# Kernel optimization log

Hardware: AMD Instinct MI355X
Metric: run time of the kernel (lower is better)

## Reference

```python
import jax, jax.numpy as jnp
import numpy as np
import math

DIM = 2048
NUM_HEADS = 16
HEAD_DIM = DIM // NUM_HEADS
SEQ = 2048
BATCH = 4
THETA = 10000.0


def _rope_tables(seq_len, d, theta):
    # faithful to RotaryEmbedding: emb = cat([freqs, freqs], -1), then [..., ::2]
    inv_freq = 1.0 / theta ** (np.arange(0, d, 2, dtype=np.float32) / d)  # [d/2]
    t = np.arange(seq_len, dtype=np.float32)
    freqs = np.einsum('i,j->ij', t, inv_freq)          # [S, d/2]
    emb = np.concatenate([freqs, freqs], axis=-1)       # [S, d]
    cos_split = np.cos(emb)[:, ::2]                     # [S, d/2]
    sin_split = np.sin(emb)[:, ::2]                     # [S, d/2]
    return jnp.asarray(cos_split), jnp.asarray(sin_split)


def _apply_rope(x, cos_s, sin_s):
    # x: [b, h, s, d]; cos_s/sin_s: [s, d/2]
    x1 = x[..., ::2]
    x2 = x[..., 1::2]
    c = cos_s[None, None]
    s = sin_s[None, None]
    return jnp.concatenate([x1 * c - x2 * s, x1 * s + x2 * c], axis=-1)


def setup_inputs() -> dict:
    key = jax.random.key(0)
    k1, k2, k3 = jax.random.split(key, 3)
    x = jax.random.normal(k1, (BATCH, SEQ, DIM), dtype=jnp.float32)
    # causal additive mask [1,1,S,S]
    neg = jnp.finfo(jnp.float32).min
    causal = jnp.tril(jnp.ones((SEQ, SEQ), dtype=bool))
    mask = jnp.where(causal, 0.0, neg)[None, None].astype(jnp.float32)
    w_qkv = jax.random.normal(k2, (3 * DIM, DIM), dtype=jnp.float32) * (1.0 / math.sqrt(DIM))
    w_out = jax.random.normal(k3, (DIM, DIM), dtype=jnp.float32) * (1.0 / math.sqrt(DIM))
    return {"x": x, "mask": mask, "w_qkv": w_qkv, "w_out": w_out}


def reference(x, mask, w_qkv, w_out):
    b, s, _ = x.shape
    h, d = NUM_HEADS, HEAD_DIM
    qkv = jnp.einsum('bse,fe->bsf', x, w_qkv)           # [b, s, 3*dim]
    q, k, v = jnp.split(qkv, 3, axis=-1)
    # b s (h d) -> b h s d
    reshp = lambda t: t.reshape(b, s, h, d).transpose(0, 2, 1, 3)
    q, k, v = reshp(q), reshp(k), reshp(v)
    cos_s, sin_s = _rope_tables(s, d, THETA)
    q = _apply_rope(q, cos_s, sin_s)
    k = _apply_rope(k, cos_s, sin_s)
    att = jnp.einsum('bhqd,bhkd->bhqk', q, k) / math.sqrt(d)
    att = att + mask
    att = jax.nn.softmax(att, axis=-1)
    y = jnp.einsum('bhqk,bhkd->bhqd', att, v)           # [b, h, s, d]
    y = y.transpose(0, 2, 1, 3).reshape(b, s, h * d)
    return jnp.einsum('bse,fe->bsf', y, w_out)
```

## Files before the change

kernel.cpp:

```cpp
#include <hip/hip_runtime.h>

typedef unsigned short u16;
typedef unsigned int u32;
typedef __attribute__((ext_vector_type(4))) float f32x4;
typedef __attribute__((ext_vector_type(16))) float f32x16;
typedef __attribute__((ext_vector_type(8))) short bf16x8;
typedef __attribute__((ext_vector_type(4))) float float4v;
typedef __attribute__((ext_vector_type(4))) unsigned short u16x4;
typedef __attribute__((ext_vector_type(8))) unsigned short u16x8;

__device__ __forceinline__ float bf2f(u16 u) { return __uint_as_float(((u32)u) << 16); }
__device__ __forceinline__ u16 f2bf(float f) {
  u32 x = __float_as_uint(f);
  x += 0x7fffu + ((x >> 16) & 1u);
  return (u16)(x >> 16);
}
__device__ __forceinline__ u32 cvtpk(float lo, float hi_) {
  u32 r;
  asm("v_cvt_pk_bf16_f32 %0, %1, %2" : "=v"(r) : "v"(lo), "v"(hi_));
  return r;
}

__device__ __forceinline__ void gll16(const void* g, void* l) {
  __builtin_amdgcn_global_load_lds((const __attribute__((address_space(1))) void*)g,
                                   (__attribute__((address_space(3))) void*)l, 16, 0, 0);
}

#define MFMA_BF16(a, b, c) __builtin_amdgcn_mfma_f32_16x16x32_bf16((a), (b), (c), 0, 0, 0)
#define MFMA32(a, b, c) __builtin_amdgcn_mfma_f32_32x32x16_bf16((a), (b), (c), 0, 0, 0)

#define BARRIER() __builtin_amdgcn_s_barrier()
#define VMCNT(n) asm volatile("s_waitcnt vmcnt(" #n ")" ::: "memory")

__global__ __launch_bounds__(256) void cast_kernel(const float* __restrict__ src,
                                                   u16* __restrict__ dst, int n) {
  const int stride = gridDim.x * 256 * 4;
  for (int i = (blockIdx.x * 256 + threadIdx.x) * 4; i < n; i += stride) {
    const float4v v = *(const float4v*)(src + i);
    u16x4 o;
    o[0] = f2bf(v[0]); o[1] = f2bf(v[1]); o[2] = f2bf(v[2]); o[3] = f2bf(v[3]);
    *(u16x4*)(dst + i) = o;
  }
}

__global__ __launch_bounds__(256) void rope_tables(float* __restrict__ cosd,
                                                   float* __restrict__ sind) {
  const int idx = blockIdx.x * 256 + threadIdx.x;
  const int t = idx >> 6, j = idx & 63;
  const float inv = powf(10000.0f, -(float)(j & 31) * (1.0f / 32.0f));
  const float ang = (float)t * inv;
  cosd[idx] = cosf(ang);
  sind[idx] = sinf(ang);
}

#define PH_MFMA(MG, NG, BF)                                                      \
  do {                                                                           \
    _Pragma("unroll") for (int i_ = 0; i_ < 4; ++i_)                             \
      _Pragma("unroll") for (int jn_ = 0; jn_ < 2; ++jn_)                        \
        _Pragma("unroll") for (int ks_ = 0; ks_ < 2; ++ks_)                      \
          acc[(MG) * 4 + i_][(NG) * 2 + jn_] =                                   \
              MFMA_BF16(af[i_][ks_], BF[jn_][ks_],                               \
                        acc[(MG) * 4 + i_][(NG) * 2 + jn_]);                     \
  } while (0)

#define LDB_M(bb, ng, BF)                                                        \
  do {                                                                           \
    const char* base_ = (const char*)&LDS[bb][1][ng][0];                         \
    _Pragma("unroll") for (int jn_ = 0; jn_ < 2; ++jn_) {                        \
      const int R_ = jn_ * 64 + wc * 16 + l15;                                   \
      _Pragma("unroll") for (int ks_ = 0; ks_ < 2; ++ks_)                        \
        BF[jn_][ks_] = *(const bf16x8*)(base_ + R_ * 128 +                       \
                                        ((ks_ * 64 + l4 * 16) ^ ((R_ & 7) << 4)));\
    }                                                                            \
  } while (0)

template <int MODE>
__global__ __launch_bounds__(512, 2) void gemm_bt8(const u16* __restrict__ A,
                                                   const u16* __restrict__ B,
                                                   void* __restrict__ Cv, int M, int N, int K,
                                                   int lda, int ldb, int ldc) {
  __shared__ __align__(16) u16 LDS[2][2][2][128 * 64];
  const int nbn = N >> 8;
  const int nwg = gridDim.x;
  const int wg = (blockIdx.x & 7) * (nwg >> 3) + (blockIdx.x >> 3);
  const int bm = wg / nbn, bn = wg % nbn;
  const int tid = threadIdx.x;
  const int w = tid >> 6, l = tid & 63, l15 = l & 15, l4 = l >> 4;
  const int wr = w >> 2, wc = w & 3;
  const u16* Abase = A + (size_t)bm * 256 * lda;
  const u16* Bbase = B + (size_t)bn * 256 * ldb;
  const int NT = K >> 6;

  f32x4 acc[8][4] = {};
  bf16x8 af[4][2], bfr0[2][2], bfr1[2][2];

  auto STAGE = [&](int sel, int h, int t) {
    const u16* src = (sel ? Bbase + (size_t)h * 128 * ldb : Abase + (size_t)h * 128 * lda) +
                     t * 64;
    const int ld = sel ? ldb : lda;
    char* dst = (char*)&LDS[t & 1][sel][h][0];
#pragma unroll
    for (int j = 0; j < 2; ++j) {
      const int o = j * 8192 + tid * 16;
      const int r = o >> 7;
      const int cb = (o & 127) ^ ((r & 7) << 4);
      gll16(src + (size_t)r * ld + (cb >> 1), dst + o);
    }
  };
  auto LDA_ = [&](int bb, int mg) {
    const char* base = (const char*)&LDS[bb][0][mg][0];
#pragma unroll
    for (int i = 0; i < 4; ++i) {
      const int R = i * 32 + wr * 16 + l15;
#pragma unroll
      for (int ks = 0; ks < 2; ++ks)
        af[i][ks] = *(const bf16x8*)(base + R * 128 + ((ks * 64 + l4 * 16) ^ ((R & 7) << 4)));
    }
  };

  STAGE(0, 0, 0); STAGE(1, 0, 0); STAGE(0, 1, 0); STAGE(1, 1, 0);
  if (NT > 1) { STAGE(1, 0, 1); STAGE(1, 1, 1); STAGE(0, 1, 1); }
  VMCNT(6);
  BARRIER();

  for (int T = 0; T < NT; ++T) {
    const int bb = T & 1;
    LDA_(bb, 0); LDB_M(bb, 0, bfr0);
    if (T + 1 < NT) STAGE(0, 0, T + 1);
    BARRIER();
    __builtin_amdgcn_s_setprio(1); PH_MFMA(0, 0, bfr0); __builtin_amdgcn_s_setprio(0);
    BARRIER();
    LDB_M(bb, 1, bfr1);
    if (T + 2 < NT) STAGE(1, 0, T + 2);
    BARRIER();
    __builtin_amdgcn_s_setprio(1); PH_MFMA(0, 1, bfr1); __builtin_amdgcn_s_setprio(0);
    BARRIER();
    LDA_(bb, 1);
    if (T + 2 < NT) STAGE(1, 1, T + 2);
    BARRIER();
    __builtin_amdgcn_s_setprio(1); PH_MFMA(1, 1, bfr1); __builtin_amdgcn_s_setprio(0);
    BARRIER();
    if (T + 2 < NT) STAGE(0, 1, T + 2);
    BARRIER();
    __builtin_amdgcn_s_setprio(1); PH_MFMA(1, 0, bfr0); __builtin_amdgcn_s_setprio(0);
    if (T + 2 < NT) { VMCNT(6); } else { VMCNT(0); }
    BARRIER();
  }

#pragma unroll
  for (int mf = 0; mf < 8; ++mf) {
    const int mg = mf >> 2, i = mf & 3;
    const int row0 = bm * 256 + mg * 128 + i * 32 + wr * 16 + l4 * 4;
#pragma unroll
    for (int f = 0; f < 4; ++f) {
      const int col = bn * 256 + f * 64 + wc * 16 + l15;
      const f32x4 a = acc[mf][f];
      if (MODE == 0) {
        float* C = (float*)Cv;
#pragma unroll
        for (int r = 0; r < 4; ++r)
          C[(size_t)(row0 + r) * ldc + col] = a[r];
      } else if (bn < 16) {
        u16* C = (u16*)Cv;
#pragma unroll
        for (int r = 0; r < 4; ++r)
          C[(size_t)(row0 + r) * 6144 + col] = f2bf(a[r]);
      } else {
        u16* C = (u16*)Cv;
        const int batch = row0 >> 11;
        const int s0 = row0 & 2047;
        const int vcol = col - 4096;
        u16* vb = C + (size_t)((batch * 16 + (vcol >> 7)) * 128 + (vcol & 127)) * 6144 +
                  4096 + s0;
        union { u32 u[2]; u16x4 v; } pk;
        pk.u[0] = cvtpk(a[0], a[1]);
        pk.u[1] = cvtpk(a[2], a[3]);
        *(u16x4*)vb = pk.v;
      }
    }
  }
}

__global__ __launch_bounds__(256) void rope_apply_inplace(u16* __restrict__ qkvb,
                                                          const float* __restrict__ cosd,
                                                          const float* __restrict__ sind) {
  const int wid = blockIdx.x * 4 + (threadIdx.x >> 6);
  const int j = threadIdx.x & 63;
  const int h = wid & 15;
  const int m = wid >> 4;
  const int s = m & 2047;
  const float c = cosd[s * 64 + j];
  const float sn = sind[s * 64 + j];
  u16* qp = qkvb + (size_t)m * 6144 + h * 128;
  u16* kp = qp + 2048;
  const u32 qv = *(const u32*)(qp + 2 * j);
  const u32 kv = *(const u32*)(kp + 2 * j);
  const float q1 = bf2f((u16)(qv & 0xffff)), q2 = bf2f((u16)(qv >> 16));
  const float k1 = bf2f((u16)(kv & 0xffff)), k2 = bf2f((u16)(kv >> 16));
  qp[j]      = f2bf(q1 * c - q2 * sn);
  qp[64 + j] = f2bf(q1 * sn + q2 * c);
  kp[j]      = f2bf(k1 * c - k2 * sn);
  kp[64 + j] = f2bf(k1 * sn + k2 * c);
}

__global__ __launch_bounds__(512, 2) void flash_attn(u16* __restrict__ qkvb) {
  __shared__ __align__(16) char smem[65536];
  const int bh = blockIdx.x;
  const int qt = 7 - blockIdx.y;
  const int b = bh >> 4, h = bh & 15;
  const int tid = threadIdx.x;
  const int w = tid >> 6, l = tid & 63;
  const int l31 = l & 31, hi = l >> 5;

  const int q0 = qt * 256 + w * 32;
  const int qg = q0 + l31;

  bf16x8 qf[8];
  {
    const u16* Qrow = qkvb + (size_t)(b * 2048 + qg) * 6144 + h * 128 + hi * 8;
#pragma unroll
    for (int d = 0; d < 8; ++d) qf[d] = *(const bf16x8*)(Qrow + d * 16);
  }

  f32x16 ot[4];
#pragma unroll
  for (int dt = 0; dt < 4; ++dt) ot[dt] = 0.f;
  float mrun = -1e30f, lrun = 0.f;

  const int NT = 4 * qt + 4;
  const u16* Kg0 = qkvb + (size_t)b * 2048 * 6144 + 2048 + h * 128;
  const u16* Vg0 = qkvb + (size_t)bh * 128 * 6144 + 4096;

  auto STAGE = [&](int t) {
    const u16* Kg = Kg0 + (size_t)t * 64 * 6144;
    const u16* Vg = Vg0 + t * 64;
    char* kd = smem + (t & 1) * 16384;
    char* vd = smem + 32768 + (t & 1) * 16384;
#pragma unroll
    for (int j = 0; j < 2; ++j) {
      const int o = j * 8192 + tid * 16;
      {
        const int r = o >> 8;
        const int cb = (o & 255) ^ ((r & 15) << 4);
        gll16(Kg + (size_t)r * 6144 + (cb >> 1), kd + o);
      }
      {
        const int r = o >> 7;
        const int cb = (o & 127) ^ ((r & 7) << 4);
        gll16(Vg + (size_t)r * 6144 + (cb >> 1), vd + o);
      }
    }
  };

  STAGE(0);
  VMCNT(0);
  BARRIER();

  for (int kt = 0; kt < NT; ++kt) {
    if (kt + 1 < NT) STAGE(kt + 1);

    if (kt * 64 <= q0 + 31) {
      const char* Kb = smem + (kt & 1) * 16384;
      const char* Vb = smem + 32768 + (kt & 1) * 16384;

      f32x16 sa[2];
      sa[0] = 0.f; sa[1] = 0.f;
#pragma unroll
      for (int ks2 = 0; ks2 < 2; ++ks2) {
        const int R = ks2 * 32 + l31;
#pragma unroll
        for (int d = 0; d < 8; ++d) {
          const bf16x8 kf = *(const bf16x8*)(Kb + R * 256 +
                                             ((d * 32 + hi * 16) ^ ((R & 15) << 4)));
          sa[ks2] = MFMA32(kf, qf[d], sa[ks2]);
        }
      }

      const float SCALE = 0.08838834764831845f;
      float tmax = -1e30f;
      if (kt * 64 + 63 > q0) {
#pragma unroll
        for (int ks2 = 0; ks2 < 2; ++ks2)
#pragma unroll
          for (int rg = 0; rg < 16; ++rg) {
            const int key = kt * 64 + ks2 * 32 + (rg & 3) + 8 * (rg >> 2) + 4 * hi;
            float sv = sa[ks2][rg] * SCALE;
            sv = (key > qg) ? -1e30f : sv;
            sa[ks2][rg] = sv;
            tmax = fmaxf(tmax, sv);
          }
      } else {
#pragma unroll
        for (int ks2 = 0; ks2 < 2; ++ks2)
#pragma unroll
          for (int rg = 0; rg < 16; ++rg) {
            const float sv = sa[ks2][rg] * SCALE;
            sa[ks2][rg] = sv;
            tmax = fmaxf(tmax, sv);
          }
      }
      tmax = fmaxf(tmax, __shfl_xor(tmax, 32));

      const float mnew = fmaxf(mrun, tmax);
      const float alpha = __expf(mrun - mnew);
      mrun = mnew;
      float rsum = 0.f;
#pragma unroll
      for (int ks2 = 0; ks2 < 2; ++ks2)
#pragma unroll
        for (int rg = 0; rg < 16; ++rg) {
          const float pv = __expf(sa[ks2][rg] - mnew);
          sa[ks2][rg] = pv;
          rsum += pv;
        }
      rsum += __shfl_xor(rsum, 32);
      lrun = lrun * alpha + rsum;
#pragma unroll
      for (int dt = 0; dt < 4; ++dt)
#pragma unroll
        for (int rg = 0; rg < 16; ++rg) ot[dt][rg] *= alpha;

      bf16x8 pfrag[4];
#pragma unroll
      for (int t = 0; t < 4; ++t) {
        const int ks2 = t >> 1;
        const int gA = 2 * (t & 1);
        const int gB = gA + 1;
        const u32 a0 = cvtpk(sa[ks2][gA * 4 + 0], sa[ks2][gA * 4 + 1]);
        const u32 a1 = cvtpk(sa[ks2][gA * 4 + 2], sa[ks2][gA * 4 + 3]);
        const u32 b0 = cvtpk(sa[ks2][gB * 4 + 0], sa[ks2][gB * 4 + 1]);
        const u32 b1 = cvtpk(sa[ks2][gB * 4 + 2], sa[ks2][gB * 4 + 3]);
        const u32 snd0 = hi ? a0 : b0;
        const u32 snd1 = hi ? a1 : b1;
        const u32 rcv0 = (u32)__shfl_xor((int)snd0, 32);
        const u32 rcv1 = (u32)__shfl_xor((int)snd1, 32);
        union { u32 u[4]; bf16x8 v; } pk;
        pk.u[0] = hi ? rcv0 : a0;
        pk.u[1] = hi ? rcv1 : a1;
        pk.u[2] = hi ? b0 : rcv0;
        pk.u[3] = hi ? b1 : rcv1;
        pfrag[t] = pk.v;
      }

#pragma unroll
      for (int dt = 0; dt < 4; ++dt) {
        const int R = dt * 32 + l31;
#pragma unroll
        for (int t = 0; t < 4; ++t) {
          const bf16x8 vf = *(const bf16x8*)(Vb + R * 128 +
                                             ((t * 32 + hi * 16) ^ ((R & 7) << 4)));
          ot[dt] = MFMA32(vf, pfrag[t], ot[dt]);
        }
      }
    }

    VMCNT(0);
    BARRIER();
  }

  const float inv = 1.0f / lrun;
  char* E = smem + w * 8192;
#pragma unroll
  for (int dt = 0; dt < 4; ++dt)
#pragma unroll
    for (int rp = 0; rp < 8; ++rp) {
      const int rg = 2 * rp;
      const int d0 = dt * 32 + (rg & 3) + 8 * (rg >> 2) + 4 * hi;
      const u32 pkv = cvtpk(ot[dt][rg] * inv, ot[dt][rg + 1] * inv);
      *(u32*)(E + l31 * 256 + ((d0 * 2) ^ ((l31 & 15) << 4))) = pkv;
    }
#pragma unroll
  for (int p = 0; p < 8; ++p) {
    const int q = p * 4 + (l >> 4);
    const int c = l & 15;
    const bf16x8 vv = *(const bf16x8*)(E + q * 256 + ((c * 16) ^ ((q & 15) << 4)));
    *(bf16x8*)(qkvb + (size_t)(b * 2048 + q0 + q) * 6144 + h * 128 + c * 8) = vv;
  }
}

extern "C" void kernel_launch(void* const* d_in, const int* in_sizes, int n_in,
                              void* d_out, int out_size, void* d_ws, size_t ws_size,
                              hipStream_t stream) {
  const float* x     = (const float*)d_in[0];
  const float* w_qkv = (const float*)d_in[2];
  const float* w_out = (const float*)d_in[3];
  float* out = (float*)d_out;
  char* ws = (char*)d_ws;

  u16* woutb = (u16*)(ws);
  u16* xb    = (u16*)(ws + ((size_t)8 << 20));
  u16* wqkvb = (u16*)(ws + ((size_t)40 << 20));
  u16* qkvb  = (u16*)(ws + ((size_t)64 << 20));
  float* cosd = (float*)(ws + ((size_t)160 << 20));
  float* sind = (float*)(ws + ((size_t)160 << 20) + ((size_t)1 << 19));

  cast_kernel<<<2048, 256, 0, stream>>>(x, xb, 8192 * 2048);
  cast_kernel<<<2048, 256, 0, stream>>>(w_qkv, wqkvb, 6144 * 2048);
  cast_kernel<<<1024, 256, 0, stream>>>(w_out, woutb, 2048 * 2048);
  rope_tables<<<512, 256, 0, stream>>>(cosd, sind);
  gemm_bt8<1><<<768, 512, 0, stream>>>(xb, wqkvb, qkvb, 8192, 6144, 2048,
                                       2048, 2048, 6144);
  rope_apply_inplace<<<32768, 256, 0, stream>>>(qkvb, cosd, sind);
  flash_attn<<<dim3(64, 8), 512, 0, stream>>>(qkvb);
  gemm_bt8<0><<<256, 512, 0, stream>>>(qkvb, woutb, out, 8192, 2048, 2048,
                                       6144, 2048, 2048);
}
```

Before: 415.1 us.

## Fuse RoPE into QKV GEMM epilogue and unroll K loop by two

Removes the separate rope_apply_inplace kernel and applies the rotary embedding in the QKV GEMM epilogue, using a lane shuffle to pair even and odd columns and writing the results into the split-half layout. The GEMM main loop is also unrolled by two k-tiles, so LDS buffer indices are compile-time constants rather than computed from T&1. This saves a full read-modify-write pass over Q and K, at the cost of scattered epilogue stores and cos/sin loads inside the GEMM. The unrolled loop and the unconditional prologue assume NT is even and at least 2.

```diff
diff --git a/kernel.cpp b/kernel.cpp
--- a/kernel.cpp
+++ b/kernel.cpp
@@ -30,6 +30,7 @@
 #define MFMA32(a, b, c) __builtin_amdgcn_mfma_f32_32x32x16_bf16((a), (b), (c), 0, 0, 0)
 
 #define BARRIER() __builtin_amdgcn_s_barrier()
+#define SETP(n) __builtin_amdgcn_s_setprio(n)
 #define VMCNT(n) asm volatile("s_waitcnt vmcnt(" #n ")" ::: "memory")
 
 __global__ __launch_bounds__(256) void cast_kernel(const float* __restrict__ src,
@@ -74,11 +75,30 @@
     }                                                                            \
   } while (0)
 
+#define KTILE(BB, OB, TT)                                                        \
+  do {                                                                           \
+    LDA_(BB, 0); LDB_M(BB, 0, bfr0);                                            \
+    if ((TT) + 1 < NT) STAGE(OB, 0, 0, (TT) + 1);                                \
+    BARRIER(); SETP(1); PH_MFMA(0, 0, bfr0); SETP(0); BARRIER();                 \
+    LDB_M(BB, 1, bfr1);                                                          \
+    if ((TT) + 2 < NT) STAGE(BB, 1, 0, (TT) + 2);                                \
+    BARRIER(); SETP(1); PH_MFMA(0, 1, bfr1); SETP(0); BARRIER();                 \
+    LDA_(BB, 1);                                                                 \
+    if ((TT) + 2 < NT) STAGE(BB, 1, 1, (TT) + 2);                                \
+    BARRIER(); SETP(1); PH_MFMA(1, 1, bfr1); SETP(0); BARRIER();                 \
+    if ((TT) + 2 < NT) STAGE(BB, 0, 1, (TT) + 2);                                \
+    BARRIER(); SETP(1); PH_MFMA(1, 0, bfr0); SETP(0);                            \
+    if ((TT) + 2 < NT) { VMCNT(6); } else { VMCNT(0); }                          \
+    BARRIER();                                                                   \
+  } while (0)
+
 template <int MODE>
 __global__ __launch_bounds__(512, 2) void gemm_bt8(const u16* __restrict__ A,
                                                    const u16* __restrict__ B,
                                                    void* __restrict__ Cv, int M, int N, int K,
-                                                   int lda, int ldb, int ldc) {
+                                                   int lda, int ldb, int ldc,
+                                                   const float* __restrict__ cosd,
+                                                   const float* __restrict__ sind) {
   __shared__ __align__(16) u16 LDS[2][2][2][128 * 64];
   const int nbn = N >> 8;
   const int nwg = gridDim.x;
@@ -94,11 +114,11 @@
   f32x4 acc[8][4] = {};
   bf16x8 af[4][2], bfr0[2][2], bfr1[2][2];
 
-  auto STAGE = [&](int sel, int h, int t) {
+  auto STAGE = [&](int buf, int sel, int h, int t) {
     const u16* src = (sel ? Bbase + (size_t)h * 128 * ldb : Abase + (size_t)h * 128 * lda) +
                      t * 64;
     const int ld = sel ? ldb : lda;
-    char* dst = (char*)&LDS[t & 1][sel][h][0];
+    char* dst = (char*)&LDS[buf][sel][h][0];
 #pragma unroll
     for (int j = 0; j < 2; ++j) {
       const int o = j * 8192 + tid * 16;
@@ -118,33 +138,14 @@
     }
   };
 
-  STAGE(0, 0, 0); STAGE(1, 0, 0); STAGE(0, 1, 0); STAGE(1, 1, 0);
-  if (NT > 1) { STAGE(1, 0, 1); STAGE(1, 1, 1); STAGE(0, 1, 1); }
+  STAGE(0, 0, 0, 0); STAGE(0, 1, 0, 0); STAGE(0, 0, 1, 0); STAGE(0, 1, 1, 0);
+  STAGE(1, 1, 0, 1); STAGE(1, 1, 1, 1); STAGE(1, 0, 1, 1);
   VMCNT(6);
   BARRIER();
 
-  for (int T = 0; T < NT; ++T) {
-    const int bb = T & 1;
-    LDA_(bb, 0); LDB_M(bb, 0, bfr0);
-    if (T + 1 < NT) STAGE(0, 0, T + 1);
-    BARRIER();
-    __builtin_amdgcn_s_setprio(1); PH_MFMA(0, 0, bfr0); __builtin_amdgcn_s_setprio(0);
-    BARRIER();
-    LDB_M(bb, 1, bfr1);
-    if (T + 2 < NT) STAGE(1, 0, T + 2);
-    BARRIER();
-    __builtin_amdgcn_s_setprio(1); PH_MFMA(0, 1, bfr1); __builtin_amdgcn_s_setprio(0);
-    BARRIER();
-    LDA_(bb, 1);
-    if (T + 2 < NT) STAGE(1, 1, T + 2);
-    BARRIER();
-    __builtin_amdgcn_s_setprio(1); PH_MFMA(1, 1, bfr1); __builtin_amdgcn_s_setprio(0);
-    BARRIER();
-    if (T + 2 < NT) STAGE(0, 1, T + 2);
-    BARRIER();
-    __builtin_amdgcn_s_setprio(1); PH_MFMA(1, 0, bfr0); __builtin_amdgcn_s_setprio(0);
-    if (T + 2 < NT) { VMCNT(6); } else { VMCNT(0); }
-    BARRIER();
+  for (int T = 0; T < NT; T += 2) {
+    KTILE(0, 1, T);
+    KTILE(1, 0, T + 1);
   }
 
 #pragma unroll
@@ -162,9 +163,22 @@
           C[(size_t)(row0 + r) * ldc + col] = a[r];
       } else if (bn < 16) {
         u16* C = (u16*)Cv;
-#pragma unroll
-        for (int r = 0; r < 4; ++r)
-          C[(size_t)(row0 + r) * 6144 + col] = f2bf(a[r]);
+        const int hc = (f * 64 + wc * 16 + l15) & 127;
+        const int jj = hc >> 1;
+        const int odd = hc & 1;
+        const int co = (col & ~127) + jj + (odd << 6);
+#pragma unroll
+        for (int r = 0; r < 4; ++r) {
+          const int row = row0 + r;
+          const int seq = row & 2047;
+          const float v = a[r];
+          const float p = __shfl_xor(v, 1);
+          const float cv = cosd[seq * 64 + jj];
+          const float sv = sind[seq * 64 + jj];
+          const float res = odd ? (p * sv + v * cv)
+                                : (v * cv - p * sv);
+          C[(size_t)row * 6144 + co] = f2bf(res);
+        }
       } else {
         u16* C = (u16*)Cv;
         const int batch = row0 >> 11;
@@ -179,28 +193,6 @@
       }
     }
   }
-}
-
-__global__ __launch_bounds__(256) void rope_apply_inplace(u16* __restrict__ qkvb,
-                                                          const float* __restrict__ cosd,
-                                                          const float* __restrict__ sind) {
-  const int wid = blockIdx.x * 4 + (threadIdx.x >> 6);
-  const int j = threadIdx.x & 63;
-  const int h = wid & 15;
-  const int m = wid >> 4;
-  const int s = m & 2047;
-  const float c = cosd[s * 64 + j];
-  const float sn = sind[s * 64 + j];
-  u16* qp = qkvb + (size_t)m * 6144 + h * 128;
-  u16* kp = qp + 2048;
-  const u32 qv = *(const u32*)(qp + 2 * j);
-  const u32 kv = *(const u32*)(kp + 2 * j);
-  const float q1 = bf2f((u16)(qv & 0xffff)), q2 = bf2f((u16)(qv >> 16));
-  const float k1 = bf2f((u16)(kv & 0xffff)), k2 = bf2f((u16)(kv >> 16));
-  qp[j]      = f2bf(q1 * c - q2 * sn);
-  qp[64 + j] = f2bf(q1 * sn + q2 * c);
-  kp[j]      = f2bf(k1 * c - k2 * sn);
-  kp[64 + j] = f2bf(k1 * sn + k2 * c);
 }
 
 __global__ __launch_bounds__(512, 2) void flash_attn(u16* __restrict__ qkvb) {
@@ -399,9 +391,8 @@
   cast_kernel<<<1024, 256, 0, stream>>>(w_out, woutb, 2048 * 2048);
   rope_tables<<<512, 256, 0, stream>>>(cosd, sind);
   gemm_bt8<1><<<768, 512, 0, stream>>>(xb, wqkvb, qkvb, 8192, 6144, 2048,
-                                       2048, 2048, 6144);
-  rope_apply_inplace<<<32768, 256, 0, stream>>>(qkvb, cosd, sind);
+                                       2048, 2048, 6144, cosd, sind);
   flash_attn<<<dim3(64, 8), 512, 0, stream>>>(qkvb);
   gemm_bt8<0><<<256, 512, 0, stream>>>(qkvb, woutb, out, 8192, 2048, 2048,
-                                       6144, 2048, 2048);
-}
+                                       6144, 2048, 2048, nullptr, nullptr);
+}
```

Result: no change. 413.1 us (-0.5%).
